# Performance work log

Hardware: AMD Instinct MI355X
Metric: run time of the kernel (lower is better)

## Reference

```python
import jax, jax.numpy as jnp
import numpy as np


def _cayley(X):
    # torch orthogonal parametrization, orthogonal_map='cayley', use_trivialization=False:
    # A = tril(X,-1); A = A - A^T (skew);  Q = (I - A/2)^{-1} (I + A/2)
    n = X.shape[0]
    A = jnp.tril(X, -1)
    A = A - A.T
    I = jnp.eye(n, dtype=X.dtype)
    return jnp.linalg.solve(I - 0.5 * A, I + 0.5 * A)


def setup_inputs() -> dict:
    key = jax.random.key(0)
    ks = jax.random.split(key, 8)
    L, R = 64, 64
    B, S = 4, 2048
    x = jax.random.normal(ks[0], (B, S, L * R), dtype=jnp.float32)
    return {
        "x": x,
        "u_left": jax.random.normal(ks[1], (L, L), dtype=jnp.float32) * 0.02,
        "v_left": jax.random.normal(ks[2], (L, L), dtype=jnp.float32) * 0.02,
        "diag_left": jnp.ones((L,), dtype=jnp.float32),
        "u_right": jax.random.normal(ks[3], (R, R), dtype=jnp.float32) * 0.02,
        "v_right": jax.random.normal(ks[4], (R, R), dtype=jnp.float32) * 0.02,
        "diag_right": jnp.ones((R,), dtype=jnp.float32),
        "diag_scale": 1.0 + 0.01 * jax.random.normal(ks[5], (L * R,), dtype=jnp.float32),
    }


def reference(x, u_left, v_left, diag_left, u_right, v_right, diag_right, diag_scale):
    L = diag_left.shape[0]
    R = diag_right.shape[0]
    # SVD-composed trans matrices: M = Cayley(U) @ diag(S) @ Cayley(V)
    m_left = _cayley(u_left) @ (diag_left[:, None] * _cayley(v_left))    # [L, L]
    m_right = _cayley(u_right) @ (diag_right[:, None] * _cayley(v_right))  # [R, R]
    # add_diag: elementwise diagonal scale on hidden dim
    xs = x * diag_scale
    shp = xs.shape
    xm = xs.reshape(-1, L, R)  # [N, L, R]
    # kronecker_matmul: m_left^T @ X @ m_right
    out = jnp.einsum('il,nij,jr->nlr', m_left, xm, m_right)
    return out.reshape(shp)
```

## Files before the change

kernel.cpp:

```cpp
#include <hip/hip_runtime.h>
#include <hip/hip_bf16.h>

typedef __attribute__((ext_vector_type(8))) short short8;
typedef __attribute__((ext_vector_type(4))) short short4v;
typedef __attribute__((ext_vector_type(4))) float floatx4;

#define MFMA(a, b, c) __builtin_amdgcn_mfma_f32_16x16x32_bf16((a), (b), (c), 0, 0, 0)

#define BARRIER_LDS() asm volatile("s_waitcnt lgkmcnt(0)\n\ts_barrier" ::: "memory")

__device__ __forceinline__ short f2bf(float f) {
    unsigned u = __float_as_uint(f);
    u += 0x7fffu + ((u >> 16) & 1u);
    return (short)(u >> 16);
}

__device__ __forceinline__ short8 pack_bf16(floatx4 a, floatx4 b) {
    short8 r;
    r[0] = f2bf(a.x); r[1] = f2bf(a.y); r[2] = f2bf(a.z); r[3] = f2bf(a.w);
    r[4] = f2bf(b.x); r[5] = f2bf(b.y); r[6] = f2bf(b.z); r[7] = f2bf(b.w);
    return r;
}

__device__ void cayley64(const float* __restrict__ X, const float* __restrict__ dg,
                         short* outArr, int mode,
                         short* Brow, float* Bcol, short* T0, short* T1, int tid)
{
    int i0 = (tid * 16) >> 6;
    int j0 = (tid * 16) & 63;
#pragma unroll
    for (int s = 0; s < 16; ++s) {
        int i = i0, j = j0 + s;
        float b = 0.f;
        if (i > j)      b =  0.5f * X[i * 64 + j];
        else if (i < j) b = -0.5f * X[j * 64 + i];
        Brow[i * 72 + j] = f2bf(b);
        Bcol[j * 68 + i] = b;
        T0[j * 72 + i]   = f2bf(b);
    }
    __syncthreads();

    int lane = tid & 63, w = tid >> 6, m = lane & 15, q = lane >> 4;
    int arow = (w * 16 + m) * 72;
    short8 a0 = *(const short8*)&Brow[arow + q * 8];
    short8 a1 = *(const short8*)&Brow[arow + 32 + q * 8];

    short* Tbuf[2] = {T0, T1};
    int cur = 0;
    const int NSTEP = 6;
    for (int step = 0; step < NSTEP; ++step) {
        bool last = (step == NSTEP - 1);
        short* Tr = Tbuf[cur];
        short* Tw = Tbuf[cur ^ 1];
#pragma unroll
        for (int c = 0; c < 4; ++c) {
            int coff = c * 16 + m;
            short8 b0 = *(const short8*)&Tr[coff * 72 + q * 8];
            short8 b1 = *(const short8*)&Tr[coff * 72 + 32 + q * 8];
            floatx4 acc = {0.f, 0.f, 0.f, 0.f};
            acc = MFMA(a0, b0, acc);
            acc = MFMA(a1, b1, acc);
            int row0 = w * 16 + q * 4;
            floatx4 badd = *(const floatx4*)&Bcol[coff * 68 + row0];
            floatx4 t = badd + acc;
            if (!last) {
                short4v pk = { f2bf(t.x), f2bf(t.y), f2bf(t.z), f2bf(t.w) };
                *(short4v*)&Tw[coff * 72 + row0] = pk;
            } else {
                int col = coff;
                floatx4 cv;
                cv.x = ((row0 + 0) == col ? 1.f : 0.f) + 2.f * t.x;
                cv.y = ((row0 + 1) == col ? 1.f : 0.f) + 2.f * t.y;
                cv.z = ((row0 + 2) == col ? 1.f : 0.f) + 2.f * t.z;
                cv.w = ((row0 + 3) == col ? 1.f : 0.f) + 2.f * t.w;
                if (mode == 0) {
                    outArr[(row0 + 0) * 72 + col] = f2bf(cv.x);
                    outArr[(row0 + 1) * 72 + col] = f2bf(cv.y);
                    outArr[(row0 + 2) * 72 + col] = f2bf(cv.z);
                    outArr[(row0 + 3) * 72 + col] = f2bf(cv.w);
                } else {
                    floatx4 dv = *(const floatx4*)&dg[row0];
                    short4v pk = { f2bf(cv.x * dv.x), f2bf(cv.y * dv.y),
                                   f2bf(cv.z * dv.z), f2bf(cv.w * dv.w) };
                    *(short4v*)&outArr[col * 72 + row0] = pk;
                }
            }
        }
        __syncthreads();
        cur ^= 1;
    }
}

__global__ __launch_bounds__(256) void k_prep(
        const float* __restrict__ u_l, const float* __restrict__ v_l, const float* __restrict__ dg_l,
        const float* __restrict__ u_r, const float* __restrict__ v_r, const float* __restrict__ dg_r,
        short* __restrict__ wsOut)
{
    __shared__ __align__(16) short Brow[64 * 72];
    __shared__ __align__(16) float Bcol[64 * 68];
    __shared__ __align__(16) short T0[64 * 72];
    __shared__ __align__(16) short T1[64 * 72];
    __shared__ __align__(16) short CvA[64 * 72];
    __shared__ __align__(16) short CuB[64 * 72];

    int tid = threadIdx.x;
    const float* U  = (blockIdx.x == 0) ? u_l  : u_r;
    const float* V  = (blockIdx.x == 0) ? v_l  : v_r;
    const float* DG = (blockIdx.x == 0) ? dg_l : dg_r;
    short* outT = wsOut + blockIdx.x * 4096;

    cayley64(V, DG, CvA, 1, Brow, Bcol, T0, T1, tid);
    __syncthreads();
    cayley64(U, DG, CuB, 0, Brow, Bcol, T0, T1, tid);
    __syncthreads();

    int lane = tid & 63, w = tid >> 6, m = lane & 15, q = lane >> 4;
    int arow = (w * 16 + m) * 72;
    short8 a0 = *(const short8*)&CvA[arow + q * 8];
    short8 a1 = *(const short8*)&CvA[arow + 32 + q * 8];
#pragma unroll
    for (int c = 0; c < 4; ++c) {
        short8 b0 = *(const short8*)&CuB[(c * 16 + m) * 72 + q * 8];
        short8 b1 = *(const short8*)&CuB[(c * 16 + m) * 72 + 32 + q * 8];
        floatx4 acc = {0.f, 0.f, 0.f, 0.f};
        acc = MFMA(a0, b0, acc);
        acc = MFMA(a1, b1, acc);
        int row0 = w * 16 + q * 4, col = c * 16 + m;
        outT[(row0 + 0) * 64 + col] = f2bf(acc.x);
        outT[(row0 + 1) * 64 + col] = f2bf(acc.y);
        outT[(row0 + 2) * 64 + col] = f2bf(acc.z);
        outT[(row0 + 3) * 64 + col] = f2bf(acc.w);
    }
}

#define NPB 4

__global__ __launch_bounds__(256) void k_main(
        const float* __restrict__ x, const float* __restrict__ dsc,
        const short* __restrict__ mLT, const short* __restrict__ mRT,
        float* __restrict__ out, int N)
{
    __shared__ __align__(16) short ST[2][64 * 72];

    int tid = threadIdx.x;
    int lane = tid & 63, w = tid >> 6, m = lane & 15, q = lane >> 4;
    const int rowoff = (w * 16 + m) * 64 + q * 8;

    floatx4 ds0a = *(const floatx4*)&dsc[rowoff];
    floatx4 ds0b = *(const floatx4*)&dsc[rowoff + 4];
    floatx4 ds1a = *(const floatx4*)&dsc[rowoff + 32];
    floatx4 ds1b = *(const floatx4*)&dsc[rowoff + 36];

    short8 pf0 = *(const short8*)&mLT[(w * 16 + m) * 64 + q * 8];
    short8 pf1 = *(const short8*)&mLT[(w * 16 + m) * 64 + 32 + q * 8];
    short8 qf[4][2];
#pragma unroll
    for (int c = 0; c < 4; ++c) {
        qf[c][0] = *(const short8*)&mRT[(c * 16 + m) * 64 + q * 8];
        qf[c][1] = *(const short8*)&mRT[(c * 16 + m) * 64 + 32 + q * 8];
    }

    const int base = blockIdx.x * NPB;
    const float* xb = x + (size_t)base * 4096 + rowoff;

    floatx4 xr0, xr1, xr2, xr3;
    if (base < N) {
        xr0 = *(const floatx4*)&xb[0];
        xr1 = *(const floatx4*)&xb[4];
        xr2 = *(const floatx4*)&xb[32];
        xr3 = *(const floatx4*)&xb[36];
    }

#pragma unroll
    for (int it = 0; it < NPB; ++it) {
        int n = base + it;
        if (n >= N) break;

        floatx4 nx0, nx1, nx2, nx3;
        bool pf = (it + 1 < NPB) && (n + 1 < N);
        if (pf) {
            const float* xn = xb + (size_t)(it + 1) * 4096;
            nx0 = *(const floatx4*)&xn[0];
            nx1 = *(const floatx4*)&xn[4];
            nx2 = *(const floatx4*)&xn[32];
            nx3 = *(const floatx4*)&xn[36];
        }

        short8 xa0 = pack_bf16(xr0 * ds0a, xr1 * ds0b);
        short8 xa1 = pack_bf16(xr2 * ds1a, xr3 * ds1b);

        short* STw = ST[it & 1];
#pragma unroll
        for (int c = 0; c < 4; ++c) {
            floatx4 s = {0.f, 0.f, 0.f, 0.f};
            s = MFMA(xa0, qf[c][0], s);
            s = MFMA(xa1, qf[c][1], s);
            short4v pk = { f2bf(s.x), f2bf(s.y), f2bf(s.z), f2bf(s.w) };
            *(short4v*)&STw[(c * 16 + m) * 72 + w * 16 + q * 4] = pk;
        }
        BARRIER_LDS();

        float* op = out + (size_t)n * 4096;
#pragma unroll
        for (int c = 0; c < 4; ++c) {
            short8 sb0 = *(const short8*)&STw[(c * 16 + m) * 72 + q * 8];
            short8 sb1 = *(const short8*)&STw[(c * 16 + m) * 72 + 32 + q * 8];
            floatx4 o = {0.f, 0.f, 0.f, 0.f};
            o = MFMA(pf0, sb0, o);
            o = MFMA(pf1, sb1, o);
            int row0 = w * 16 + q * 4, col = c * 16 + m;
            op[(row0 + 0) * 64 + col] = o.x;
            op[(row0 + 1) * 64 + col] = o.y;
            op[(row0 + 2) * 64 + col] = o.z;
            op[(row0 + 3) * 64 + col] = o.w;
        }
        if (pf) { xr0 = nx0; xr1 = nx1; xr2 = nx2; xr3 = nx3; }
    }
}

extern "C" void kernel_launch(void* const* d_in, const int* in_sizes, int n_in,
                              void* d_out, int out_size, void* d_ws, size_t ws_size,
                              hipStream_t stream) {
    const float* x    = (const float*)d_in[0];
    const float* u_l  = (const float*)d_in[1];
    const float* v_l  = (const float*)d_in[2];
    const float* dg_l = (const float*)d_in[3];
    const float* u_r  = (const float*)d_in[4];
    const float* v_r  = (const float*)d_in[5];
    const float* dg_r = (const float*)d_in[6];
    const float* dsc  = (const float*)d_in[7];
    float* out = (float*)d_out;
    short* ws  = (short*)d_ws;

    int N = in_sizes[0] / 4096;

    hipLaunchKernelGGL(k_prep, dim3(2), dim3(256), 0, stream,
                       u_l, v_l, dg_l, u_r, v_r, dg_r, ws);
    int grid = (N + NPB - 1) / NPB;
    hipLaunchKernelGGL(k_main, dim3(grid), dim3(256), 0, stream,
                       x, dsc, ws, ws + 4096, out, N);
}
```

Before: 263.3 us.

## Give each wavefront whole matrices to remove block barriers

Each wavefront now processes complete 64x64 matrices (two per wave) using a private LDS tile. Previously four waves cooperated on one matrix and had to synchronise with a block barrier. All left and right factor fragments are held in registers, diag_scale is reloaded per row-tile, and outputs use nontemporal stores. The intent is to drop s_barrier stalls and to bypass the cache on write-back, at the cost of more registers and LDS per block and less parallelism per matrix.

New measurement: 271.5 us. +3.1%, slower.

```diff
diff --git a/kernel.cpp b/kernel.cpp
--- a/kernel.cpp
+++ b/kernel.cpp
@@ -6,8 +6,6 @@
 typedef __attribute__((ext_vector_type(4))) float floatx4;
 
 #define MFMA(a, b, c) __builtin_amdgcn_mfma_f32_16x16x32_bf16((a), (b), (c), 0, 0, 0)
-
-#define BARRIER_LDS() asm volatile("s_waitcnt lgkmcnt(0)\n\ts_barrier" ::: "memory")
 
 __device__ __forceinline__ short f2bf(float f) {
     unsigned u = __float_as_uint(f);
@@ -133,88 +131,94 @@
     }
 }
 
-#define NPB 4
+#define MPW 2
 
 __global__ __launch_bounds__(256) void k_main(
         const float* __restrict__ x, const float* __restrict__ dsc,
         const short* __restrict__ mLT, const short* __restrict__ mRT,
         float* __restrict__ out, int N)
 {
-    __shared__ __align__(16) short ST[2][64 * 72];
-
-    int tid = threadIdx.x;
-    int lane = tid & 63, w = tid >> 6, m = lane & 15, q = lane >> 4;
-    const int rowoff = (w * 16 + m) * 64 + q * 8;
-
-    floatx4 ds0a = *(const floatx4*)&dsc[rowoff];
-    floatx4 ds0b = *(const floatx4*)&dsc[rowoff + 4];
-    floatx4 ds1a = *(const floatx4*)&dsc[rowoff + 32];
-    floatx4 ds1b = *(const floatx4*)&dsc[rowoff + 36];
-
-    short8 pf0 = *(const short8*)&mLT[(w * 16 + m) * 64 + q * 8];
-    short8 pf1 = *(const short8*)&mLT[(w * 16 + m) * 64 + 32 + q * 8];
-    short8 qf[4][2];
-#pragma unroll
-    for (int c = 0; c < 4; ++c) {
-        qf[c][0] = *(const short8*)&mRT[(c * 16 + m) * 64 + q * 8];
-        qf[c][1] = *(const short8*)&mRT[(c * 16 + m) * 64 + 32 + q * 8];
-    }
-
-    const int base = blockIdx.x * NPB;
-    const float* xb = x + (size_t)base * 4096 + rowoff;
-
-    floatx4 xr0, xr1, xr2, xr3;
-    if (base < N) {
-        xr0 = *(const floatx4*)&xb[0];
-        xr1 = *(const floatx4*)&xb[4];
-        xr2 = *(const floatx4*)&xb[32];
-        xr3 = *(const floatx4*)&xb[36];
-    }
-
-#pragma unroll
-    for (int it = 0; it < NPB; ++it) {
-        int n = base + it;
-        if (n >= N) break;
-
-        floatx4 nx0, nx1, nx2, nx3;
-        bool pf = (it + 1 < NPB) && (n + 1 < N);
-        if (pf) {
-            const float* xn = xb + (size_t)(it + 1) * 4096;
-            nx0 = *(const floatx4*)&xn[0];
-            nx1 = *(const floatx4*)&xn[4];
-            nx2 = *(const floatx4*)&xn[32];
-            nx3 = *(const floatx4*)&xn[36];
+    __shared__ __align__(16) short ST[4][64 * 72];
+
+    const int tid = threadIdx.x;
+    const int w = tid >> 6, lane = tid & 63, m = lane & 15, q = lane >> 4;
+    short* st = ST[w];
+
+    short8 pf[4][2], qf[4][2];
+#pragma unroll
+    for (int r = 0; r < 4; ++r) {
+        pf[r][0] = *(const short8*)&mLT[(r * 16 + m) * 64 + q * 8];
+        pf[r][1] = *(const short8*)&mLT[(r * 16 + m) * 64 + 32 + q * 8];
+        qf[r][0] = *(const short8*)&mRT[(r * 16 + m) * 64 + q * 8];
+        qf[r][1] = *(const short8*)&mRT[(r * 16 + m) * 64 + 32 + q * 8];
+    }
+
+    const int gw = blockIdx.x * 4 + w;
+    const long n0 = (long)gw * MPW;
+    if (n0 >= N) return;
+    const int nmat = ((long)N - n0 >= MPW) ? MPW : (int)((long)N - n0);
+    const int nch  = nmat * 4;
+
+    const int loff = m * 64 + q * 8;
+    const float* xw = x + (size_t)n0 * 4096 + loff;
+    float* ow = out + (size_t)n0 * 4096;
+
+    floatx4 cx0 = *(const floatx4*)&xw[0];
+    floatx4 cx1 = *(const floatx4*)&xw[4];
+    floatx4 cx2 = *(const floatx4*)&xw[32];
+    floatx4 cx3 = *(const floatx4*)&xw[36];
+
+    for (int i = 0; i < nmat; ++i) {
+#pragma unroll
+        for (int rt = 0; rt < 4; ++rt) {
+            const int cc = i * 4 + rt;
+            const bool pfok = (cc + 1 < nch);
+            floatx4 nx0, nx1, nx2, nx3;
+            if (pfok) {
+                const float* xn = xw + (size_t)(cc + 1) * 1024;
+                nx0 = *(const floatx4*)&xn[0];
+                nx1 = *(const floatx4*)&xn[4];
+                nx2 = *(const floatx4*)&xn[32];
+                nx3 = *(const floatx4*)&xn[36];
+            }
+            const float* dp = dsc + rt * 1024 + loff;
+            floatx4 d0 = *(const floatx4*)&dp[0];
+            floatx4 d1 = *(const floatx4*)&dp[4];
+            floatx4 d2 = *(const floatx4*)&dp[32];
+            floatx4 d3 = *(const floatx4*)&dp[36];
+
+            short8 a0 = pack_bf16(cx0 * d0, cx1 * d1);
+            short8 a1 = pack_bf16(cx2 * d2, cx3 * d3);
+
+#pragma unroll
+            for (int c = 0; c < 4; ++c) {
+                floatx4 s = {0.f, 0.f, 0.f, 0.f};
+                s = MFMA(a0, qf[c][0], s);
+                s = MFMA(a1, qf[c][1], s);
+                short4v pk = { f2bf(s.x), f2bf(s.y), f2bf(s.z), f2bf(s.w) };
+                *(short4v*)&st[(c * 16 + m) * 72 + rt * 16 + q * 4] = pk;
+            }
+            if (pfok) { cx0 = nx0; cx1 = nx1; cx2 = nx2; cx3 = nx3; }
         }
 
-        short8 xa0 = pack_bf16(xr0 * ds0a, xr1 * ds0b);
-        short8 xa1 = pack_bf16(xr2 * ds1a, xr3 * ds1b);
-
-        short* STw = ST[it & 1];
-#pragma unroll
-        for (int c = 0; c < 4; ++c) {
-            floatx4 s = {0.f, 0.f, 0.f, 0.f};
-            s = MFMA(xa0, qf[c][0], s);
-            s = MFMA(xa1, qf[c][1], s);
-            short4v pk = { f2bf(s.x), f2bf(s.y), f2bf(s.z), f2bf(s.w) };
-            *(short4v*)&STw[(c * 16 + m) * 72 + w * 16 + q * 4] = pk;
+        float* op = ow + (size_t)i * 4096;
+#pragma unroll
+        for (int c2 = 0; c2 < 4; ++c2) {
+            short8 b0 = *(const short8*)&st[(c2 * 16 + m) * 72 + q * 8];
+            short8 b1 = *(const short8*)&st[(c2 * 16 + m) * 72 + 32 + q * 8];
+            const int col = c2 * 16 + m;
+#pragma unroll
+            for (int r = 0; r < 4; ++r) {
+                floatx4 o = {0.f, 0.f, 0.f, 0.f};
+                o = MFMA(pf[r][0], b0, o);
+                o = MFMA(pf[r][1], b1, o);
+                const int row0 = r * 16 + q * 4;
+                __builtin_nontemporal_store(o.x, &op[(row0 + 0) * 64 + col]);
+                __builtin_nontemporal_store(o.y, &op[(row0 + 1) * 64 + col]);
+                __builtin_nontemporal_store(o.z, &op[(row0 + 2) * 64 + col]);
+                __builtin_nontemporal_store(o.w, &op[(row0 + 3) * 64 + col]);
+            }
         }
-        BARRIER_LDS();
-
-        float* op = out + (size_t)n * 4096;
-#pragma unroll
-        for (int c = 0; c < 4; ++c) {
-            short8 sb0 = *(const short8*)&STw[(c * 16 + m) * 72 + q * 8];
-            short8 sb1 = *(const short8*)&STw[(c * 16 + m) * 72 + 32 + q * 8];
-            floatx4 o = {0.f, 0.f, 0.f, 0.f};
-            o = MFMA(pf0, sb0, o);
-            o = MFMA(pf1, sb1, o);
-            int row0 = w * 16 + q * 4, col = c * 16 + m;
-            op[(row0 + 0) * 64 + col] = o.x;
-            op[(row0 + 1) * 64 + col] = o.y;
-            op[(row0 + 2) * 64 + col] = o.z;
-            op[(row0 + 3) * 64 + col] = o.w;
-        }
-        if (pf) { xr0 = nx0; xr1 = nx1; xr2 = nx2; xr3 = nx3; }
     }
 }
 
@@ -236,7 +240,7 @@
 
     hipLaunchKernelGGL(k_prep, dim3(2), dim3(256), 0, stream,
                        u_l, v_l, dg_l, u_r, v_r, dg_r, ws);
-    int grid = (N + NPB - 1) / NPB;
+    int grid = (N + MPW * 4 - 1) / (MPW * 4);
     hipLaunchKernelGGL(k_main, dim3(grid), dim3(256), 0, stream,
                        x, dsc, ws, ws + 4096, out, N);
 }
```
